# Kernel optimization log

Hardware: AMD Instinct MI355X
Metric: run time of the kernel (lower is better)

Reference implementation:

```python
import jax, jax.numpy as jnp
import numpy as np

N_LAYERS = 4
BN_EPS = 1e-5


def setup_inputs() -> dict:
    key = jax.random.key(0)
    ks = jax.random.split(key, 10)
    N, E, F, H = 50000, 600000, 128, 128
    x = jax.random.normal(ks[0], (N, F), dtype=jnp.float32)
    edge_index = jax.random.randint(ks[1], (2, E), 0, N, dtype=jnp.int64)
    s = 0.05  # small init to keep deep ReLU stack numerically tame
    return {
        "x": x,
        "edge_index": edge_index,
        # stacked params for the 4 GINConv MLPs (num_features == hidden)
        "conv_w1": jax.random.normal(ks[2], (N_LAYERS, F, H), dtype=jnp.float32) * s,
        "conv_b1": jnp.zeros((N_LAYERS, H), dtype=jnp.float32),
        "conv_gamma": jnp.ones((N_LAYERS, H), dtype=jnp.float32),
        "conv_beta": jnp.zeros((N_LAYERS, H), dtype=jnp.float32),
        "conv_w2": jax.random.normal(ks[3], (N_LAYERS, H, H), dtype=jnp.float32) * s,
        "conv_b2": jnp.zeros((N_LAYERS, H), dtype=jnp.float32),
        "fc1_w": jax.random.normal(ks[4], (H, H), dtype=jnp.float32) * s,
        "fc1_b": jnp.zeros((H,), dtype=jnp.float32),
        "fc2_w": jax.random.normal(ks[5], (H, 1), dtype=jnp.float32) * s,
        "fc2_b": jnp.zeros((1,), dtype=jnp.float32),
    }


def _batchnorm(h, gamma, beta):
    # training-mode BatchNorm1d: batch stats over the node axis, biased variance
    mean = jnp.mean(h, axis=0, keepdims=True)
    var = jnp.mean(jnp.square(h - mean), axis=0, keepdims=True)
    return (h - mean) * jax.lax.rsqrt(var + BN_EPS) * gamma + beta


def _gin_layer(x, src, dst, w1, b1, gamma, beta, w2, b2):
    n = x.shape[0]
    # GIN sum aggregation with eps=0: (1+eps)*x_i + sum_{j->i} x_j
    agg = x + jax.ops.segment_sum(x[src], dst, num_segments=n)
    h = jax.nn.relu(agg @ w1 + b1)
    h = _batchnorm(h, gamma, beta)
    return jax.nn.relu(h @ w2 + b2)


def reference(x, edge_index, conv_w1, conv_b1, conv_gamma, conv_beta,
              conv_w2, conv_b2, fc1_w, fc1_b, fc2_w, fc2_b):
    src, dst = edge_index[0], edge_index[1]
    h = x
    for l in range(N_LAYERS):
        h = _gin_layer(h, src, dst, conv_w1[l], conv_b1[l], conv_gamma[l],
                       conv_beta[l], conv_w2[l], conv_b2[l])
    h = jax.nn.relu(h @ fc1_w + fc1_b)
    return h @ fc2_w + fc2_b  # [N, 1]
```

## Files before the change

kernel.cpp:

```cpp
#include <hip/hip_runtime.h>

constexpr int FEAT = 128;

typedef __attribute__((ext_vector_type(8))) _Float16 f16x8;
typedef __attribute__((ext_vector_type(4))) float f32x4;

__device__ inline unsigned int halfpair(float a, float b) {
  unsigned short ua = __builtin_bit_cast(unsigned short, (_Float16)a);
  unsigned short ub = __builtin_bit_cast(unsigned short, (_Float16)b);
  return (unsigned int)ua | ((unsigned int)ub << 16);
}
__device__ inline unsigned short halfr(float a) {
  return __builtin_bit_cast(unsigned short, (_Float16)a);
}
__device__ inline float2 halfup(unsigned int u) {
  _Float16 lo = __builtin_bit_cast(_Float16, (unsigned short)(u & 0xffffu));
  _Float16 hi = __builtin_bit_cast(_Float16, (unsigned short)(u >> 16));
  return make_float2((float)lo, (float)hi);
}

__device__ __host__ inline int kperm(int k) {
  return ((k >> 5) << 5) + (((k >> 2) & 3) << 3) + (((k >> 4) & 1) << 2) + (k & 3);
}


__global__ __launch_bounds__(256) void prep_kernel(
    const float* __restrict__ x, unsigned short* __restrict__ xb, int n4,
    const float* __restrict__ w1, const float* __restrict__ fc1w,
    unsigned short* __restrict__ wimg,
    const int* __restrict__ dst, int* __restrict__ deg, int E, int B1, int B2) {
  int bid = blockIdx.x;
  if (bid < B1) {
    int idx = bid * 256 + threadIdx.x;
    if (idx < n4) {
      float4 v = ((const float4*)x)[idx];
      uint2 o;
      o.x = halfpair(v.x, v.y);
      o.y = halfpair(v.z, v.w);
      ((uint2*)xb)[idx] = o;
    }
  } else if (bid < B1 + B2) {
    int idx = (bid - B1) * 256 + threadIdx.x;
    if (idx < 5 * FEAT * FEAT) {
      int m = idx >> 14;
      int r = idx & (FEAT * FEAT - 1);
      int k = r >> 7, n = r & 127;
      float v = (m < 4) ? w1[idx] : fc1w[r];
      int p = kperm(k);
      int slot = p >> 3, e = p & 7;
      wimg[m * FEAT * FEAT + n * FEAT + ((slot ^ (n & 7)) << 3) + e] = halfr(v);
    }
  } else {
    int e = (bid - B1 - B2) * 256 + threadIdx.x;
    if (e < E) atomicAdd(&deg[dst[e]], 1);
  }
}


__global__ __launch_bounds__(256) void scan1_kernel(const int* __restrict__ in,
                                                    int* __restrict__ bsum, int n) {
  int base = blockIdx.x * 1024 + threadIdx.x * 4;
  int s = 0;
  if (base + 3 < n) {
    int4 v = *(const int4*)(in + base);
    s = v.x + v.y + v.z + v.w;
  } else {
#pragma unroll
    for (int j = 0; j < 4; j++)
      if (base + j < n) s += in[base + j];
  }
#pragma unroll
  for (int off = 1; off < 64; off <<= 1) s += __shfl_xor(s, off);
  __shared__ int ws[4];
  int lane = threadIdx.x & 63, wid = threadIdx.x >> 6;
  if (lane == 0) ws[wid] = s;
  __syncthreads();
  if (threadIdx.x == 0) bsum[blockIdx.x] = ws[0] + ws[1] + ws[2] + ws[3];
}

__global__ __launch_bounds__(64) void scan2_kernel(int* __restrict__ bsum, int nb) {
  int t = threadIdx.x;
  int v = (t < nb) ? bsum[t] : 0;
  int s = v;
#pragma unroll
  for (int off = 1; off < 64; off <<= 1) {
    int u = __shfl_up(s, off);
    if (t >= off) s += u;
  }
  if (t < nb) bsum[t] = s - v;
}

__global__ __launch_bounds__(256) void scan3_kernel(const int* __restrict__ in,
                                                    const int* __restrict__ boff,
                                                    int* __restrict__ out,
                                                    int* __restrict__ out2, int n) {
  int t = threadIdx.x;
  int base = blockIdx.x * 1024 + t * 4;
  int v0 = 0, v1 = 0, v2 = 0, v3 = 0;
  if (base + 3 < n) {
    int4 v = *(const int4*)(in + base);
    v0 = v.x; v1 = v.y; v2 = v.z; v3 = v.w;
  } else {
    if (base + 0 < n) v0 = in[base + 0];
    if (base + 1 < n) v1 = in[base + 1];
    if (base + 2 < n) v2 = in[base + 2];
  }
  int ts = v0 + v1 + v2 + v3;
  int s = ts;
  int lane = t & 63, wid = t >> 6;
#pragma unroll
  for (int off = 1; off < 64; off <<= 1) {
    int u = __shfl_up(s, off);
    if (lane >= off) s += u;
  }
  __shared__ int ws[4];
  if (lane == 63) ws[wid] = s;
  __syncthreads();
  int cross = 0;
#pragma unroll
  for (int i = 0; i < 4; i++)
    if (i < wid) cross += ws[i];
  int excl = boff[blockIdx.x] + cross + (s - ts);
  int o0 = excl, o1 = o0 + v0, o2 = o1 + v1, o3 = o2 + v2;
  if (base + 3 < n) {
    *(int4*)(out + base) = make_int4(o0, o1, o2, o3);
    *(int4*)(out2 + base) = make_int4(o0, o1, o2, o3);
  } else {
    if (base + 0 < n) { out[base + 0] = o0; out2[base + 0] = o0; }
    if (base + 1 < n) { out[base + 1] = o1; out2[base + 1] = o1; }
    if (base + 2 < n) { out[base + 2] = o2; out2[base + 2] = o2; }
  }
}

__global__ void fill_kernel(const int* __restrict__ src, const int* __restrict__ dst,
                            int* __restrict__ cursor, int* __restrict__ col, int E) {
  int e = blockIdx.x * blockDim.x + threadIdx.x;
  if (e < E) {
    int p = atomicAdd(&cursor[dst[e]], 1);
    col[p] = src[e];
  }
}


__global__ void agg_kernel(const unsigned short* __restrict__ x, const int* __restrict__ rowptr,
                           const int* __restrict__ col, unsigned short* __restrict__ agg, int N) {
  int gid = blockIdx.x * blockDim.x + threadIdx.x;
  int wid = gid >> 6;
  int lane = threadIdx.x & 63;
  int node = wid * 4 + (lane >> 4);
  if (node >= N) return;
  int ln = lane & 15;
  const uint4* xr = (const uint4*)x;
  uint4 s = xr[(size_t)node * 16 + ln];
  float2 t0 = halfup(s.x), t1 = halfup(s.y), t2 = halfup(s.z), t3 = halfup(s.w);
  float a0 = t0.x, a1 = t0.y, a2 = t1.x, a3 = t1.y;
  float a4 = t2.x, a5 = t2.y, a6 = t3.x, a7 = t3.y;
  float b0 = 0.f, b1 = 0.f, b2 = 0.f, b3 = 0.f;
  float b4 = 0.f, b5 = 0.f, b6 = 0.f, b7 = 0.f;
  int e0 = rowptr[node], e1 = rowptr[node + 1];
  int e = e0;
  for (; e + 3 < e1; e += 4) {
    int c0 = col[e], c1 = col[e + 1], c2 = col[e + 2], c3 = col[e + 3];
    uint4 v = xr[(size_t)c0 * 16 + ln];
    uint4 u = xr[(size_t)c1 * 16 + ln];
    uint4 w = xr[(size_t)c2 * 16 + ln];
    uint4 z = xr[(size_t)c3 * 16 + ln];
    float2 f;
    f = halfup(v.x); a0 += f.x; a1 += f.y;
    f = halfup(v.y); a2 += f.x; a3 += f.y;
    f = halfup(v.z); a4 += f.x; a5 += f.y;
    f = halfup(v.w); a6 += f.x; a7 += f.y;
    f = halfup(u.x); b0 += f.x; b1 += f.y;
    f = halfup(u.y); b2 += f.x; b3 += f.y;
    f = halfup(u.z); b4 += f.x; b5 += f.y;
    f = halfup(u.w); b6 += f.x; b7 += f.y;
    f = halfup(w.x); a0 += f.x; a1 += f.y;
    f = halfup(w.y); a2 += f.x; a3 += f.y;
    f = halfup(w.z); a4 += f.x; a5 += f.y;
    f = halfup(w.w); a6 += f.x; a7 += f.y;
    f = halfup(z.x); b0 += f.x; b1 += f.y;
    f = halfup(z.y); b2 += f.x; b3 += f.y;
    f = halfup(z.z); b4 += f.x; b5 += f.y;
    f = halfup(z.w); b6 += f.x; b7 += f.y;
  }
  for (; e < e1; e++) {
    uint4 v = xr[(size_t)col[e] * 16 + ln];
    float2 f;
    f = halfup(v.x); a0 += f.x; a1 += f.y;
    f = halfup(v.y); a2 += f.x; a3 += f.y;
    f = halfup(v.z); a4 += f.x; a5 += f.y;
    f = halfup(v.w); a6 += f.x; a7 += f.y;
  }
  a0 += b0; a1 += b1; a2 += b2; a3 += b3;
  a4 += b4; a5 += b5; a6 += b6; a7 += b7;
  uint4 o;
  o.x = halfpair(a0, a1);
  o.y = halfpair(a2, a3);
  o.z = halfpair(a4, a5);
  o.w = halfpair(a6, a7);
  ((uint4*)agg)[(size_t)node * 16 + ln] = o;
}


__global__ __launch_bounds__(512, 4) void gemm_kernel(
    const unsigned short* __restrict__ A, const unsigned short* __restrict__ Wimg,
    const float* __restrict__ bias, unsigned short* __restrict__ C,
    float* __restrict__ pS, float* __restrict__ pQ, int N, int mode,
    const float* __restrict__ fc2w, const float* __restrict__ fc2b,
    float* __restrict__ outp) {
  __shared__ unsigned short Al[FEAT * FEAT];
  __shared__ float ls[FEAT], lq[FEAT];

  int tx = threadIdx.x;
  int row0 = blockIdx.x * FEAT;
  if (tx < FEAT) { ls[tx] = 0.f; lq[tx] = 0.f; }

#pragma unroll
  for (int i = 0; i < 4; i++) {
    int idx = tx + i * 512;
    int r = idx >> 4;
    int c = idx & 15;
    uint4 v = make_uint4(0u, 0u, 0u, 0u);
    if (row0 + r < N) v = ((const uint4*)(A + (size_t)(row0 + r) * FEAT))[c];
    int k0 = c << 3;
    int slotA = ((k0 >> 5) << 2) + ((k0 >> 2) & 3);
    int sub = (k0 >> 4) & 1;
    int sw = r & 7;
    *(uint2*)&Al[r * FEAT + ((slotA ^ sw) << 3) + (sub << 2)] = make_uint2(v.x, v.y);
    *(uint2*)&Al[r * FEAT + (((slotA + 1) ^ sw) << 3) + (sub << 2)] = make_uint2(v.z, v.w);
  }
  __syncthreads();

  int w = tx >> 6;
  int l = tx & 63;
  int llo = l & 15, lhi = l >> 4;
  int wr = (w >> 2) * 64;
  int wc = (w & 3) * 32;

  const unsigned short* w0p = Wimg + (size_t)(wc + llo) * FEAT;
  int m0 = (wc + llo) & 7;

  f32x4 acc[4][2];
#pragma unroll
  for (int mi = 0; mi < 4; mi++)
#pragma unroll
    for (int nj = 0; nj < 2; nj++) acc[mi][nj] = (f32x4)(0.f);

#pragma unroll
  for (int s = 0; s < 4; s++) {
    int so = (s << 2) + lhi;
    int woff = (so ^ m0) << 3;
    f16x8 wf0 = *(const f16x8*)&w0p[woff];
    f16x8 wf1 = *(const f16x8*)&w0p[16 * FEAT + woff];
    f16x8 af[4];
#pragma unroll
    for (int mi = 0; mi < 4; mi++) {
      int row = wr + mi * 16 + llo;
      af[mi] = *(const f16x8*)&Al[row * FEAT + ((so ^ (row & 7)) << 3)];
    }
#pragma unroll
    for (int mi = 0; mi < 4; mi++) {
      acc[mi][0] = __builtin_amdgcn_mfma_f32_16x16x32_f16(wf0, af[mi], acc[mi][0], 0, 0, 0);
      acc[mi][1] = __builtin_amdgcn_mfma_f32_16x16x32_f16(wf1, af[mi], acc[mi][1], 0, 0, 0);
    }
  }

  if (mode == 2) {
    float* red = ls;
    float pr[4] = {0.f, 0.f, 0.f, 0.f};
#pragma unroll
    for (int nj = 0; nj < 2; nj++) {
      int colb = wc + nj * 16 + lhi * 4;
      float4 bb = *(const float4*)&bias[colb];
      float4 fw = *(const float4*)&fc2w[colb];
#pragma unroll
      for (int mi = 0; mi < 4; mi++) {
        f32x4 v = acc[mi][nj];
        float v0 = fmaxf(v[0] + bb.x, 0.f);
        float v1 = fmaxf(v[1] + bb.y, 0.f);
        float v2 = fmaxf(v[2] + bb.z, 0.f);
        float v3 = fmaxf(v[3] + bb.w, 0.f);
        pr[mi] += v0 * fw.x + v1 * fw.y + v2 * fw.z + v3 * fw.w;
      }
    }
#pragma unroll
    for (int mi = 0; mi < 4; mi++) {
      float r = pr[mi];
      r += __shfl_xor(r, 16);
      r += __shfl_xor(r, 32);
      if (lhi == 0) atomicAdd(&red[wr + mi * 16 + llo], r);
    }
    __syncthreads();
    if (tx < FEAT) {
      int row = row0 + tx;
      if (row < N) outp[row] = red[tx] + fc2b[0];
    }
    return;
  }

#pragma unroll
  for (int nj = 0; nj < 2; nj++) {
    int colb = wc + nj * 16 + lhi * 4;
    float4 bb = *(const float4*)&bias[colb];
    float ps[4] = {0.f, 0.f, 0.f, 0.f}, pq[4] = {0.f, 0.f, 0.f, 0.f};
#pragma unroll
    for (int mi = 0; mi < 4; mi++) {
      int row = row0 + wr + mi * 16 + llo;
      f32x4 v = acc[mi][nj];
      float v0 = fmaxf(v[0] + bb.x, 0.f);
      float v1 = fmaxf(v[1] + bb.y, 0.f);
      float v2 = fmaxf(v[2] + bb.z, 0.f);
      float v3 = fmaxf(v[3] + bb.w, 0.f);
      if (row < N) {
        *(uint2*)&C[(size_t)row * FEAT + colb] = make_uint2(halfpair(v0, v1), halfpair(v2, v3));
        ps[0] += v0; ps[1] += v1; ps[2] += v2; ps[3] += v3;
        pq[0] += v0 * v0; pq[1] += v1 * v1; pq[2] += v2 * v2; pq[3] += v3 * v3;
      }
    }
    if (mode == 1) {
#pragma unroll
      for (int r = 0; r < 4; r++) {
        float s2 = ps[r], q2 = pq[r];
#pragma unroll
        for (int off = 1; off < 16; off <<= 1) {
          s2 += __shfl_xor(s2, off);
          q2 += __shfl_xor(q2, off);
        }
        if (llo == 0) {
          atomicAdd(&ls[colb + r], s2);
          atomicAdd(&lq[colb + r], q2);
        }
      }
    }
  }
  if (mode == 1) {
    __syncthreads();
    if (tx < FEAT) {
      pS[(size_t)blockIdx.x * FEAT + tx] = ls[tx];
      pQ[(size_t)blockIdx.x * FEAT + tx] = lq[tx];
    }
  }
}


__global__ __launch_bounds__(64) void stats_kernel(
    const float* __restrict__ pS, const float* __restrict__ pQ, int nblk,
    const float* __restrict__ gamma, const float* __restrict__ beta,
    float* __restrict__ scf, float* __restrict__ shf, int N) {
  int c = blockIdx.x;
  int ln = threadIdx.x;
  float s = 0.f, q = 0.f;
  for (int b = ln; b < nblk; b += 64) {
    s += pS[(size_t)b * FEAT + c];
    q += pQ[(size_t)b * FEAT + c];
  }
#pragma unroll
  for (int off = 32; off; off >>= 1) {
    s += __shfl_xor(s, off);
    q += __shfl_xor(q, off);
  }
  if (ln == 0) {
    float invN = 1.0f / (float)N;
    float mean = s * invN;
    float var = q * invN - mean * mean;
    float rstd = rsqrtf(var + 1e-5f);
    float scale = gamma[c] * rstd;
    scf[c] = scale;
    shf[c] = beta[c] - mean * scale;
  }
}


__global__ __launch_bounds__(128) void fold2_kernel(
    const float* __restrict__ scf, const float* __restrict__ shf,
    const float* __restrict__ w2, const float* __restrict__ b2,
    unsigned short* __restrict__ w2f, float* __restrict__ b2f) {
  __shared__ float red[FEAT];
  int c = blockIdx.x;
  int k = threadIdx.x;
  float wv = w2[k * FEAT + c];
  int p = kperm(k);
  int slot = p >> 3, e = p & 7;
  w2f[c * FEAT + ((slot ^ (c & 7)) << 3) + e] = halfr(scf[k] * wv);
  red[k] = shf[k] * wv;
  __syncthreads();
#pragma unroll
  for (int off = 64; off > 0; off >>= 1) {
    if (k < off) red[k] += red[k + off];
    __syncthreads();
  }
  if (k == 0) b2f[c] = b2[c] + red[0];
}


extern "C" void kernel_launch(void* const* d_in, const int* in_sizes, int n_in,
                              void* d_out, int out_size, void* d_ws, size_t ws_size,
                              hipStream_t stream) {
  const float* x     = (const float*)d_in[0];
  const int*   ei    = (const int*)d_in[1];
  const float* w1    = (const float*)d_in[2];
  const float* b1    = (const float*)d_in[3];
  const float* gamma = (const float*)d_in[4];
  const float* beta  = (const float*)d_in[5];
  const float* w2    = (const float*)d_in[6];
  const float* b2    = (const float*)d_in[7];
  const float* fc1w  = (const float*)d_in[8];
  const float* fc1b  = (const float*)d_in[9];
  const float* fc2w  = (const float*)d_in[10];
  const float* fc2b  = (const float*)d_in[11];
  float* out = (float*)d_out;

  int N = in_sizes[0] / FEAT;
  int E = in_sizes[1] / 2;
  const int* srcI = ei;
  const int* dstI = ei + E;

  int gemmBlocks = (N + FEAT - 1) / FEAT;
  int n = N + 1;
  int nb = (n + 1023) / 1024;

  size_t Nf = (size_t)N * FEAT;
  unsigned short* H = (unsigned short*)d_ws;
  unsigned short* G = H + Nf;
  unsigned short* wimg = G + Nf;
  unsigned short* w2f = wimg + 5 * FEAT * FEAT;
  float* b2f = (float*)(w2f + FEAT * FEAT);
  float* scf = b2f + FEAT;
  float* shf = scf + FEAT;
  float* pS = shf + FEAT;
  float* pQ = pS + (size_t)gemmBlocks * FEAT;
  int* deg = (int*)(pQ + (size_t)gemmBlocks * FEAT);
  int* rowptr = deg + ((n + 3) & ~3);
  int* cursor = rowptr + ((n + 3) & ~3);
  int* bsum = cursor + ((n + 3) & ~3);
  int* col = bsum + 64;

  hipMemsetAsync(deg, 0, n * sizeof(int), stream);
  int n4 = (int)(Nf / 4);
  int B1 = (n4 + 255) / 256;
  int B2 = (5 * FEAT * FEAT + 255) / 256;
  int B3 = (E + 255) / 256;
  prep_kernel<<<B1 + B2 + B3, 256, 0, stream>>>(x, H, n4, w1, fc1w, wimg, dstI, deg, E, B1, B2);

  scan1_kernel<<<nb, 256, 0, stream>>>(deg, bsum, n);
  scan2_kernel<<<1, 64, 0, stream>>>(bsum, nb);
  scan3_kernel<<<nb, 256, 0, stream>>>(deg, bsum, rowptr, cursor, n);
  fill_kernel<<<B3, 256, 0, stream>>>(srcI, dstI, cursor, col, E);

  int aggBlocks = (int)((((size_t)(N + 3) / 4) * 64 + 255) / 256);

  for (int l = 0; l < 4; l++) {
    agg_kernel<<<aggBlocks, 256, 0, stream>>>(H, rowptr, col, G, N);
    gemm_kernel<<<gemmBlocks, 512, 0, stream>>>(
        G, wimg + (size_t)l * FEAT * FEAT, b1 + (size_t)l * FEAT, G, pS, pQ, N, 1,
        nullptr, nullptr, nullptr);
    stats_kernel<<<FEAT, 64, 0, stream>>>(pS, pQ, gemmBlocks, gamma + (size_t)l * FEAT,
                                          beta + (size_t)l * FEAT, scf, shf, N);
    fold2_kernel<<<FEAT, FEAT, 0, stream>>>(scf, shf, w2 + (size_t)l * FEAT * FEAT,
                                            b2 + (size_t)l * FEAT, w2f, b2f);
    gemm_kernel<<<gemmBlocks, 512, 0, stream>>>(
        G, w2f, b2f, H, nullptr, nullptr, N, 0, nullptr, nullptr, nullptr);
  }

  gemm_kernel<<<gemmBlocks, 512, 0, stream>>>(
      H, wimg + (size_t)4 * FEAT * FEAT, fc1b, nullptr, nullptr, nullptr, N, 2,
      fc2w, fc2b, out);
}
```

Before: 386.3 us.

## Fuse neighbor aggregation into first GEMM and merge stats with weight folding

The sparse neighbor aggregation now runs inside the first GEMM kernel: each 512-thread block gathers and sums neighbor rows for its 128 nodes and writes them straight into shared memory, so the aggregated tile never goes to global memory and back. The stats and fold kernels are merged into one, with each of the 128 blocks redundantly reducing the per-block partial sums before folding BatchNorm into W2. This saves a global round trip of the aggregated features and two launches per layer. The cost is that the gather runs at the GEMM's occupancy, which may hide gather latency less well, and every fold block repeats the partial-sum reduction serially.

```diff
diff --git a/kernel.cpp b/kernel.cpp
--- a/kernel.cpp
+++ b/kernel.cpp
@@ -142,78 +142,168 @@
 }
 
 
-__global__ void agg_kernel(const unsigned short* __restrict__ x, const int* __restrict__ rowptr,
-                           const int* __restrict__ col, unsigned short* __restrict__ agg, int N) {
-  int gid = blockIdx.x * blockDim.x + threadIdx.x;
-  int wid = gid >> 6;
-  int lane = threadIdx.x & 63;
-  int node = wid * 4 + (lane >> 4);
-  if (node >= N) return;
+__global__ __launch_bounds__(512, 4) void fused1_kernel(
+    const unsigned short* __restrict__ H, const int* __restrict__ rowptr,
+    const int* __restrict__ col, const unsigned short* __restrict__ Wimg,
+    const float* __restrict__ bias, unsigned short* __restrict__ C,
+    float* __restrict__ pS, float* __restrict__ pQ, int N) {
+  __shared__ unsigned short Al[FEAT * FEAT];
+  __shared__ float ls[FEAT], lq[FEAT];
+
+  int tx = threadIdx.x;
+  int row0 = blockIdx.x * FEAT;
+  if (tx < FEAT) { ls[tx] = 0.f; lq[tx] = 0.f; }
+
+  int w = tx >> 6;
+  int lane = tx & 63;
   int ln = lane & 15;
-  const uint4* xr = (const uint4*)x;
-  uint4 s = xr[(size_t)node * 16 + ln];
-  float2 t0 = halfup(s.x), t1 = halfup(s.y), t2 = halfup(s.z), t3 = halfup(s.w);
-  float a0 = t0.x, a1 = t0.y, a2 = t1.x, a3 = t1.y;
-  float a4 = t2.x, a5 = t2.y, a6 = t3.x, a7 = t3.y;
-  float b0 = 0.f, b1 = 0.f, b2 = 0.f, b3 = 0.f;
-  float b4 = 0.f, b5 = 0.f, b6 = 0.f, b7 = 0.f;
-  int e0 = rowptr[node], e1 = rowptr[node + 1];
-  int e = e0;
-  for (; e + 3 < e1; e += 4) {
-    int c0 = col[e], c1 = col[e + 1], c2 = col[e + 2], c3 = col[e + 3];
-    uint4 v = xr[(size_t)c0 * 16 + ln];
-    uint4 u = xr[(size_t)c1 * 16 + ln];
-    uint4 w = xr[(size_t)c2 * 16 + ln];
-    uint4 z = xr[(size_t)c3 * 16 + ln];
-    float2 f;
-    f = halfup(v.x); a0 += f.x; a1 += f.y;
-    f = halfup(v.y); a2 += f.x; a3 += f.y;
-    f = halfup(v.z); a4 += f.x; a5 += f.y;
-    f = halfup(v.w); a6 += f.x; a7 += f.y;
-    f = halfup(u.x); b0 += f.x; b1 += f.y;
-    f = halfup(u.y); b2 += f.x; b3 += f.y;
-    f = halfup(u.z); b4 += f.x; b5 += f.y;
-    f = halfup(u.w); b6 += f.x; b7 += f.y;
-    f = halfup(w.x); a0 += f.x; a1 += f.y;
-    f = halfup(w.y); a2 += f.x; a3 += f.y;
-    f = halfup(w.z); a4 += f.x; a5 += f.y;
-    f = halfup(w.w); a6 += f.x; a7 += f.y;
-    f = halfup(z.x); b0 += f.x; b1 += f.y;
-    f = halfup(z.y); b2 += f.x; b3 += f.y;
-    f = halfup(z.z); b4 += f.x; b5 += f.y;
-    f = halfup(z.w); b6 += f.x; b7 += f.y;
-  }
-  for (; e < e1; e++) {
-    uint4 v = xr[(size_t)col[e] * 16 + ln];
-    float2 f;
-    f = halfup(v.x); a0 += f.x; a1 += f.y;
-    f = halfup(v.y); a2 += f.x; a3 += f.y;
-    f = halfup(v.z); a4 += f.x; a5 += f.y;
-    f = halfup(v.w); a6 += f.x; a7 += f.y;
-  }
-  a0 += b0; a1 += b1; a2 += b2; a3 += b3;
-  a4 += b4; a5 += b5; a6 += b6; a7 += b7;
-  uint4 o;
-  o.x = halfpair(a0, a1);
-  o.y = halfpair(a2, a3);
-  o.z = halfpair(a4, a5);
-  o.w = halfpair(a6, a7);
-  ((uint4*)agg)[(size_t)node * 16 + ln] = o;
+  const uint4* xr = (const uint4*)H;
+
+#pragma unroll
+  for (int it = 0; it < 4; it++) {
+    int r = it * 32 + w * 4 + (lane >> 4);
+    int node = row0 + r;
+    float a0 = 0.f, a1 = 0.f, a2 = 0.f, a3 = 0.f;
+    float a4 = 0.f, a5 = 0.f, a6 = 0.f, a7 = 0.f;
+    if (node < N) {
+      uint4 s = xr[(size_t)node * 16 + ln];
+      float2 f;
+      f = halfup(s.x); a0 = f.x; a1 = f.y;
+      f = halfup(s.y); a2 = f.x; a3 = f.y;
+      f = halfup(s.z); a4 = f.x; a5 = f.y;
+      f = halfup(s.w); a6 = f.x; a7 = f.y;
+      float b0 = 0.f, b1 = 0.f, b2 = 0.f, b3 = 0.f;
+      float b4 = 0.f, b5 = 0.f, b6 = 0.f, b7 = 0.f;
+      int e0 = rowptr[node], e1 = rowptr[node + 1];
+      int e = e0;
+      for (; e + 3 < e1; e += 4) {
+        int c0 = col[e], c1 = col[e + 1], c2 = col[e + 2], c3 = col[e + 3];
+        uint4 v = xr[(size_t)c0 * 16 + ln];
+        uint4 u = xr[(size_t)c1 * 16 + ln];
+        uint4 ww = xr[(size_t)c2 * 16 + ln];
+        uint4 z = xr[(size_t)c3 * 16 + ln];
+        f = halfup(v.x); a0 += f.x; a1 += f.y;
+        f = halfup(v.y); a2 += f.x; a3 += f.y;
+        f = halfup(v.z); a4 += f.x; a5 += f.y;
+        f = halfup(v.w); a6 += f.x; a7 += f.y;
+        f = halfup(u.x); b0 += f.x; b1 += f.y;
+        f = halfup(u.y); b2 += f.x; b3 += f.y;
+        f = halfup(u.z); b4 += f.x; b5 += f.y;
+        f = halfup(u.w); b6 += f.x; b7 += f.y;
+        f = halfup(ww.x); a0 += f.x; a1 += f.y;
+        f = halfup(ww.y); a2 += f.x; a3 += f.y;
+        f = halfup(ww.z); a4 += f.x; a5 += f.y;
+        f = halfup(ww.w); a6 += f.x; a7 += f.y;
+        f = halfup(z.x); b0 += f.x; b1 += f.y;
+        f = halfup(z.y); b2 += f.x; b3 += f.y;
+        f = halfup(z.z); b4 += f.x; b5 += f.y;
+        f = halfup(z.w); b6 += f.x; b7 += f.y;
+      }
+      for (; e < e1; e++) {
+        uint4 v = xr[(size_t)col[e] * 16 + ln];
+        f = halfup(v.x); a0 += f.x; a1 += f.y;
+        f = halfup(v.y); a2 += f.x; a3 += f.y;
+        f = halfup(v.z); a4 += f.x; a5 += f.y;
+        f = halfup(v.w); a6 += f.x; a7 += f.y;
+      }
+      a0 += b0; a1 += b1; a2 += b2; a3 += b3;
+      a4 += b4; a5 += b5; a6 += b6; a7 += b7;
+    }
+    int k0 = ln << 3;
+    int slotA = ((k0 >> 5) << 2) + ((k0 >> 2) & 3);
+    int sub = (k0 >> 4) & 1;
+    int sw = r & 7;
+    *(uint2*)&Al[r * FEAT + ((slotA ^ sw) << 3) + (sub << 2)] =
+        make_uint2(halfpair(a0, a1), halfpair(a2, a3));
+    *(uint2*)&Al[r * FEAT + (((slotA + 1) ^ sw) << 3) + (sub << 2)] =
+        make_uint2(halfpair(a4, a5), halfpair(a6, a7));
+  }
+  __syncthreads();
+
+  int llo = lane & 15, lhi = lane >> 4;
+  int wr = (w >> 2) * 64;
+  int wc = (w & 3) * 32;
+
+  const unsigned short* w0p = Wimg + (size_t)(wc + llo) * FEAT;
+  int m0 = (wc + llo) & 7;
+
+  f32x4 acc[4][2];
+#pragma unroll
+  for (int mi = 0; mi < 4; mi++)
+#pragma unroll
+    for (int nj = 0; nj < 2; nj++) acc[mi][nj] = (f32x4)(0.f);
+
+#pragma unroll
+  for (int s = 0; s < 4; s++) {
+    int so = (s << 2) + lhi;
+    int woff = (so ^ m0) << 3;
+    f16x8 wf0 = *(const f16x8*)&w0p[woff];
+    f16x8 wf1 = *(const f16x8*)&w0p[16 * FEAT + woff];
+    f16x8 af[4];
+#pragma unroll
+    for (int mi = 0; mi < 4; mi++) {
+      int row = wr + mi * 16 + llo;
+      af[mi] = *(const f16x8*)&Al[row * FEAT + ((so ^ (row & 7)) << 3)];
+    }
+#pragma unroll
+    for (int mi = 0; mi < 4; mi++) {
+      acc[mi][0] = __builtin_amdgcn_mfma_f32_16x16x32_f16(wf0, af[mi], acc[mi][0], 0, 0, 0);
+      acc[mi][1] = __builtin_amdgcn_mfma_f32_16x16x32_f16(wf1, af[mi], acc[mi][1], 0, 0, 0);
+    }
+  }
+
+#pragma unroll
+  for (int nj = 0; nj < 2; nj++) {
+    int colb = wc + nj * 16 + lhi * 4;
+    float4 bb = *(const float4*)&bias[colb];
+    float ps[4] = {0.f, 0.f, 0.f, 0.f}, pq[4] = {0.f, 0.f, 0.f, 0.f};
+#pragma unroll
+    for (int mi = 0; mi < 4; mi++) {
+      int row = row0 + wr + mi * 16 + llo;
+      f32x4 v = acc[mi][nj];
+      float v0 = fmaxf(v[0] + bb.x, 0.f);
+      float v1 = fmaxf(v[1] + bb.y, 0.f);
+      float v2 = fmaxf(v[2] + bb.z, 0.f);
+      float v3 = fmaxf(v[3] + bb.w, 0.f);
+      if (row < N) {
+        *(uint2*)&C[(size_t)row * FEAT + colb] = make_uint2(halfpair(v0, v1), halfpair(v2, v3));
+        ps[0] += v0; ps[1] += v1; ps[2] += v2; ps[3] += v3;
+        pq[0] += v0 * v0; pq[1] += v1 * v1; pq[2] += v2 * v2; pq[3] += v3 * v3;
+      }
+    }
+#pragma unroll
+    for (int r = 0; r < 4; r++) {
+      float s2 = ps[r], q2 = pq[r];
+#pragma unroll
+      for (int off = 1; off < 16; off <<= 1) {
+        s2 += __shfl_xor(s2, off);
+        q2 += __shfl_xor(q2, off);
+      }
+      if (llo == 0) {
+        atomicAdd(&ls[colb + r], s2);
+        atomicAdd(&lq[colb + r], q2);
+      }
+    }
+  }
+  __syncthreads();
+  if (tx < FEAT) {
+    pS[(size_t)blockIdx.x * FEAT + tx] = ls[tx];
+    pQ[(size_t)blockIdx.x * FEAT + tx] = lq[tx];
+  }
 }
 
 
 __global__ __launch_bounds__(512, 4) void gemm_kernel(
     const unsigned short* __restrict__ A, const unsigned short* __restrict__ Wimg,
-    const float* __restrict__ bias, unsigned short* __restrict__ C,
-    float* __restrict__ pS, float* __restrict__ pQ, int N, int mode,
+    const float* __restrict__ bias, unsigned short* __restrict__ C, int N, int mode,
     const float* __restrict__ fc2w, const float* __restrict__ fc2b,
     float* __restrict__ outp) {
   __shared__ unsigned short Al[FEAT * FEAT];
-  __shared__ float ls[FEAT], lq[FEAT];
+  __shared__ float red[FEAT];
 
   int tx = threadIdx.x;
   int row0 = blockIdx.x * FEAT;
-  if (tx < FEAT) { ls[tx] = 0.f; lq[tx] = 0.f; }
+  if (tx < FEAT) red[tx] = 0.f;
 
 #pragma unroll
   for (int i = 0; i < 4; i++) {
@@ -266,7 +356,6 @@
   }
 
   if (mode == 2) {
-    float* red = ls;
     float pr[4] = {0.f, 0.f, 0.f, 0.f};
 #pragma unroll
     for (int nj = 0; nj < 2; nj++) {
@@ -302,7 +391,6 @@
   for (int nj = 0; nj < 2; nj++) {
     int colb = wc + nj * 16 + lhi * 4;
     float4 bb = *(const float4*)&bias[colb];
-    float ps[4] = {0.f, 0.f, 0.f, 0.f}, pq[4] = {0.f, 0.f, 0.f, 0.f};
 #pragma unroll
     for (int mi = 0; mi < 4; mi++) {
       int row = row0 + wr + mi * 16 + llo;
@@ -311,78 +399,37 @@
       float v1 = fmaxf(v[1] + bb.y, 0.f);
       float v2 = fmaxf(v[2] + bb.z, 0.f);
       float v3 = fmaxf(v[3] + bb.w, 0.f);
-      if (row < N) {
+      if (row < N)
         *(uint2*)&C[(size_t)row * FEAT + colb] = make_uint2(halfpair(v0, v1), halfpair(v2, v3));
-        ps[0] += v0; ps[1] += v1; ps[2] += v2; ps[3] += v3;
-        pq[0] += v0 * v0; pq[1] += v1 * v1; pq[2] += v2 * v2; pq[3] += v3 * v3;
-      }
-    }
-    if (mode == 1) {
-#pragma unroll
-      for (int r = 0; r < 4; r++) {
-        float s2 = ps[r], q2 = pq[r];
-#pragma unroll
-        for (int off = 1; off < 16; off <<= 1) {
-          s2 += __shfl_xor(s2, off);
-          q2 += __shfl_xor(q2, off);
-        }
-        if (llo == 0) {
-          atomicAdd(&ls[colb + r], s2);
-          atomicAdd(&lq[colb + r], q2);
-        }
-      }
-    }
-  }
-  if (mode == 1) {
-    __syncthreads();
-    if (tx < FEAT) {
-      pS[(size_t)blockIdx.x * FEAT + tx] = ls[tx];
-      pQ[(size_t)blockIdx.x * FEAT + tx] = lq[tx];
-    }
-  }
-}
-
-
-__global__ __launch_bounds__(64) void stats_kernel(
+    }
+  }
+}
+
+
+__global__ __launch_bounds__(128) void statsfold_kernel(
     const float* __restrict__ pS, const float* __restrict__ pQ, int nblk,
     const float* __restrict__ gamma, const float* __restrict__ beta,
-    float* __restrict__ scf, float* __restrict__ shf, int N) {
-  int c = blockIdx.x;
-  int ln = threadIdx.x;
-  float s = 0.f, q = 0.f;
-  for (int b = ln; b < nblk; b += 64) {
-    s += pS[(size_t)b * FEAT + c];
-    q += pQ[(size_t)b * FEAT + c];
-  }
-#pragma unroll
-  for (int off = 32; off; off >>= 1) {
-    s += __shfl_xor(s, off);
-    q += __shfl_xor(q, off);
-  }
-  if (ln == 0) {
-    float invN = 1.0f / (float)N;
-    float mean = s * invN;
-    float var = q * invN - mean * mean;
-    float rstd = rsqrtf(var + 1e-5f);
-    float scale = gamma[c] * rstd;
-    scf[c] = scale;
-    shf[c] = beta[c] - mean * scale;
-  }
-}
-
-
-__global__ __launch_bounds__(128) void fold2_kernel(
-    const float* __restrict__ scf, const float* __restrict__ shf,
     const float* __restrict__ w2, const float* __restrict__ b2,
-    unsigned short* __restrict__ w2f, float* __restrict__ b2f) {
+    unsigned short* __restrict__ w2f, float* __restrict__ b2f, int N) {
   __shared__ float red[FEAT];
   int c = blockIdx.x;
   int k = threadIdx.x;
+  float S = 0.f, Q = 0.f;
+  for (int b = 0; b < nblk; b++) {
+    S += pS[(size_t)b * FEAT + k];
+    Q += pQ[(size_t)b * FEAT + k];
+  }
+  float invN = 1.0f / (float)N;
+  float mean = S * invN;
+  float var = Q * invN - mean * mean;
+  float rstd = rsqrtf(var + 1e-5f);
+  float scale = gamma[k] * rstd;
+  float shift = beta[k] - mean * scale;
   float wv = w2[k * FEAT + c];
   int p = kperm(k);
   int slot = p >> 3, e = p & 7;
-  w2f[c * FEAT + ((slot ^ (c & 7)) << 3) + e] = halfr(scf[k] * wv);
-  red[k] = shf[k] * wv;
+  w2f[c * FEAT + ((slot ^ (c & 7)) << 3) + e] = halfr(scale * wv);
+  red[k] = shift * wv;
   __syncthreads();
 #pragma unroll
   for (int off = 64; off > 0; off >>= 1) {
@@ -425,9 +472,7 @@
   unsigned short* wimg = G + Nf;
   unsigned short* w2f = wimg + 5 * FEAT * FEAT;
   float* b2f = (float*)(w2f + FEAT * FEAT);
-  float* scf = b2f + FEAT;
-  float* shf = scf + FEAT;
-  float* pS = shf + FEAT;
+  float* pS = b2f + FEAT;
   float* pQ = pS + (size_t)gemmBlocks * FEAT;
   int* deg = (int*)(pQ + (size_t)gemmBlocks * FEAT);
   int* rowptr = deg + ((n + 3) & ~3);
@@ -447,22 +492,19 @@
   scan3_kernel<<<nb, 256, 0, stream>>>(deg, bsum, rowptr, cursor, n);
   fill_kernel<<<B3, 256, 0, stream>>>(srcI, dstI, cursor, col, E);
 
-  int aggBlocks = (int)((((size_t)(N + 3) / 4) * 64 + 255) / 256);
-
   for (int l = 0; l < 4; l++) {
-    agg_kernel<<<aggBlocks, 256, 0, stream>>>(H, rowptr, col, G, N);
-    gemm_kernel<<<gemmBlocks, 512, 0, stream>>>(
-        G, wimg + (size_t)l * FEAT * FEAT, b1 + (size_t)l * FEAT, G, pS, pQ, N, 1,
-        nullptr, nullptr, nullptr);
-    stats_kernel<<<FEAT, 64, 0, stream>>>(pS, pQ, gemmBlocks, gamma + (size_t)l * FEAT,
-                                          beta + (size_t)l * FEAT, scf, shf, N);
-    fold2_kernel<<<FEAT, FEAT, 0, stream>>>(scf, shf, w2 + (size_t)l * FEAT * FEAT,
-                                            b2 + (size_t)l * FEAT, w2f, b2f);
-    gemm_kernel<<<gemmBlocks, 512, 0, stream>>>(
-        G, w2f, b2f, H, nullptr, nullptr, N, 0, nullptr, nullptr, nullptr);
-  }
-
-  gemm_kernel<<<gemmBlocks, 512, 0, stream>>>(
-      H, wimg + (size_t)4 * FEAT * FEAT, fc1b, nullptr, nullptr, nullptr, N, 2,
-      fc2w, fc2b, out);
-}
+    fused1_kernel<<<gemmBlocks, 512, 0, stream>>>(
+        H, rowptr, col, wimg + (size_t)l * FEAT * FEAT, b1 + (size_t)l * FEAT,
+        G, pS, pQ, N);
+    statsfold_kernel<<<FEAT, FEAT, 0, stream>>>(pS, pQ, gemmBlocks,
+                                                gamma + (size_t)l * FEAT,
+                                                beta + (size_t)l * FEAT,
+                                                w2 + (size_t)l * FEAT * FEAT,
+                                                b2 + (size_t)l * FEAT, w2f, b2f, N);
+    gemm_kernel<<<gemmBlocks, 512, 0, stream>>>(G, w2f, b2f, H, N, 0,
+                                                nullptr, nullptr, nullptr);
+  }
+
+  gemm_kernel<<<gemmBlocks, 512, 0, stream>>>(H, wimg + (size_t)4 * FEAT * FEAT, fc1b,
+                                              nullptr, N, 2, fc2w, fc2b, out);
+}
```

New measurement: 767.1 us. 1.99x slower.
